# Optimization experiments

Hardware: AMD Instinct MI355X
Metric: run time of the kernel (lower is better)

## Reference

```python
import jax, jax.numpy as jnp
import numpy as np

IMPOSSIBLE = -10000.0
TAGSET_SIZE = 64
NUM_TAGS = TAGSET_SIZE + 2  # C = 66
START_IDX = NUM_TAGS - 2
STOP_IDX = NUM_TAGS - 1
B, L, D = 32, 1024, 1024


def setup_inputs() -> dict:
    key = jax.random.key(0)
    k1, k2, k3, k4, k5 = jax.random.split(key, 5)
    features = jax.random.normal(k1, (B, L, D), dtype=jnp.float32)
    ys = jax.random.randint(k2, (B, L), 0, TAGSET_SIZE).astype(jnp.int64)
    masks = jnp.ones((B, L), dtype=jnp.float32)
    fc_w = jax.random.normal(k3, (D, NUM_TAGS), dtype=jnp.float32) / np.sqrt(D)
    fc_b = jax.random.normal(k4, (NUM_TAGS,), dtype=jnp.float32) * 0.01
    transitions = jax.random.normal(k5, (NUM_TAGS, NUM_TAGS), dtype=jnp.float32)
    # transitions TO start and FROM stop are impossible (torch indexing [to, from])
    transitions = transitions.at[START_IDX, :].set(IMPOSSIBLE)
    transitions = transitions.at[:, STOP_IDX].set(IMPOSSIBLE)
    return {"features": features, "ys": ys, "masks": masks,
            "fc_w": fc_w, "fc_b": fc_b, "transitions": transitions}


def _forward_algorithm(feats, masks, transitions):
    """CRF partition function. feats: [B,L,C], masks: [B,L] -> [B]."""
    Bb, Ll, C = feats.shape
    scores0 = jnp.full((Bb, C), IMPOSSIBLE, dtype=feats.dtype).at[:, START_IDX].set(0.0)

    def step(scores, xs):
        emit_t, m_t = xs  # emit_t: [B,C], m_t: [B]
        # score_t[b, j] = logsumexp_i( scores[b,i] + trans[j,i] + emit[b,j] )
        score_t = jax.nn.logsumexp(
            scores[:, None, :] + transitions[None, :, :] + emit_t[:, :, None], axis=-1)
        scores = score_t * m_t[:, None] + scores * (1.0 - m_t[:, None])
        return scores, None

    xs = (jnp.swapaxes(feats, 0, 1), jnp.swapaxes(masks, 0, 1))  # [L,B,C], [L,B]
    scores, _ = jax.lax.scan(step, scores0, xs)
    return jax.nn.logsumexp(scores + transitions[STOP_IDX][None, :], axis=-1)


def _score_sentence(feats, tags, masks, transitions):
    """Score of the gold tag path. feats: [B,L,C], tags: [B,L] -> [B]."""
    Bb, Ll, C = feats.shape
    emit = jnp.take_along_axis(feats, tags[:, :, None], axis=2)[:, :, 0]  # [B,L]
    start = jnp.full((Bb, 1), START_IDX, dtype=tags.dtype)
    tags_ext = jnp.concatenate([start, tags], axis=1)  # [B,L+1]
    trans_sc = transitions[tags_ext[:, 1:], tags_ext[:, :-1]]  # [B,L]
    lengths = masks.sum(1).astype(jnp.int32)  # [B]
    last_tag = tags_ext[jnp.arange(Bb), lengths]  # [B]
    last_score = transitions[STOP_IDX, last_tag]
    return ((trans_sc + emit) * masks).sum(1) + last_score


def reference(features, ys, masks, fc_w, fc_b, transitions):
    feats = jnp.einsum('bld,dc->blc', features, fc_w) + fc_b  # [B,L,C]
    masks_ = masks.astype(feats.dtype)
    forward_score = _forward_algorithm(feats, masks_, transitions)  # [B]
    gold_score = _score_sentence(feats, ys.astype(jnp.int32), masks_, transitions)  # [B]
    return (forward_score, gold_score)
```

## Files before the change

kernel.cpp:

```cpp
#include <hip/hip_runtime.h>
#include <hip/hip_bf16.h>
#include <stdint.h>


#define START_IDX 64
#define STOP_IDX 65
#define LN2F 0.6931471805599453f

typedef __attribute__((ext_vector_type(4))) float f32x4;
typedef __attribute__((ext_vector_type(8))) __bf16 bf16x8;
typedef __attribute__((ext_vector_type(4))) __bf16 bf16x4;

template <int CTRL>
__device__ __forceinline__ float dpp_mov(float v) {
  return __int_as_float(
      __builtin_amdgcn_update_dpp(0, __float_as_int(v), CTRL, 0xF, 0xF, true));
}
__device__ __forceinline__ float wave_max64(float v) {
  v = fmaxf(v, dpp_mov<0xB1>(v));
  v = fmaxf(v, dpp_mov<0x4E>(v));
  v = fmaxf(v, dpp_mov<0x141>(v));
  v = fmaxf(v, dpp_mov<0x140>(v));
  v = fmaxf(v, dpp_mov<0x142>(v));
  v = fmaxf(v, dpp_mov<0x143>(v));
  return v;
}
__device__ __forceinline__ float wave_sum64(float v) {
  v += dpp_mov<0xB1>(v);
  v += dpp_mov<0x4E>(v);
  v += dpp_mov<0x141>(v);
  v += dpp_mov<0x140>(v);
  v += dpp_mov<0x142>(v);
  v += dpp_mov<0x143>(v);
  return v;
}

__global__ void crf_wcvt(const float* __restrict__ W,
                         unsigned short* __restrict__ Wbt) {
  const int idx = blockIdx.x * 256 + threadIdx.x;
  const int n = idx >> 10, k = idx & 1023;
  union { __bf16 h; unsigned short u; } cv;
  cv.h = (__bf16)W[k * 66 + n];
  Wbt[idx] = cv.u;
}

__global__ __launch_bounds__(256) void crf_fwd(const float* __restrict__ features,
                                               const unsigned short* __restrict__ Wbt,
                                               const float* __restrict__ bias,
                                               const float* __restrict__ masks,
                                               const float* __restrict__ trans,
                                               float* __restrict__ featsOut,
                                               float* __restrict__ chunkP,
                                               int* __restrict__ chunkExp) {
  __shared__ __align__(16) float expE[64][64];
  __shared__ __align__(16) unsigned short T[2][4096];
  __shared__ float wmax[2][4];
  const int tid = threadIdx.x;
  const int w = tid >> 6, lane = tid & 63, g = lane >> 4, q = lane & 15;
  const int c = blockIdx.x, b = blockIdx.y;

  for (int idx = tid; idx < 4096; idx += 256) {
    const int n = idx >> 6, mm = idx & 63;
    const int off = n * 128 + ((2 * mm) ^ ((n & 7) << 4));
    *(unsigned short*)((char*)T[0] + off) =
        (n == mm) ? (unsigned short)0x3F80 : (unsigned short)0;
  }
  if (tid < 4) wmax[0][tid] = 1.0f;

  {
    const int trow = (c << 6) + 16 * w + q;
    const float* Arow = features + ((size_t)b << 20) + (size_t)trow * 1024 + 8 * g;
    const unsigned short* Bp0 = Wbt + (q + 0) * 1024 + 8 * g;
    const unsigned short* Bp1 = Wbt + (q + 16) * 1024 + 8 * g;
    const unsigned short* Bp2 = Wbt + (q + 32) * 1024 + 8 * g;
    const unsigned short* Bp3 = Wbt + (q + 48) * 1024 + 8 * g;
    f32x4 acc0 = {0.f, 0.f, 0.f, 0.f}, acc1 = acc0, acc2 = acc0, acc3 = acc0;
#pragma unroll
    for (int k0 = 0; k0 < 1024; k0 += 32) {
      float4 a0 = *(const float4*)(Arow + k0);
      float4 a1 = *(const float4*)(Arow + k0 + 4);
      bf16x8 af;
      af[0] = (__bf16)a0.x; af[1] = (__bf16)a0.y; af[2] = (__bf16)a0.z; af[3] = (__bf16)a0.w;
      af[4] = (__bf16)a1.x; af[5] = (__bf16)a1.y; af[6] = (__bf16)a1.z; af[7] = (__bf16)a1.w;
      bf16x8 b0 = *(const bf16x8*)(Bp0 + k0);
      bf16x8 b1 = *(const bf16x8*)(Bp1 + k0);
      bf16x8 b2 = *(const bf16x8*)(Bp2 + k0);
      bf16x8 b3 = *(const bf16x8*)(Bp3 + k0);
      acc0 = __builtin_amdgcn_mfma_f32_16x16x32_bf16(af, b0, acc0, 0, 0, 0);
      acc1 = __builtin_amdgcn_mfma_f32_16x16x32_bf16(af, b1, acc1, 0, 0, 0);
      acc2 = __builtin_amdgcn_mfma_f32_16x16x32_bf16(af, b2, acc2, 0, 0, 0);
      acc3 = __builtin_amdgcn_mfma_f32_16x16x32_bf16(af, b3, acc3, 0, 0, 0);
    }
    const float bb0 = bias[q + 0], bb1 = bias[q + 16];
    const float bb2 = bias[q + 32], bb3 = bias[q + 48];
#pragma unroll
    for (int r = 0; r < 4; ++r) {
      const int tl = 16 * w + 4 * g + r;
      float* orow = featsOut + (((size_t)(b << 10) + (c << 6) + tl) << 6) + q;
      const float v0 = acc0[r] + bb0, v1 = acc1[r] + bb1;
      const float v2 = acc2[r] + bb2, v3 = acc3[r] + bb3;
      orow[0] = v0; orow[16] = v1; orow[32] = v2; orow[48] = v3;
      expE[tl][q + 0]  = __expf(v0);
      expE[tl][q + 16] = __expf(v1);
      expE[tl][q + 32] = __expf(v2);
      expE[tl][q + 48] = __expf(v3);
    }
  }

  bf16x8 Ea0, Ea1;
  {
    const int i = 16 * w + q;
    const float* tp0 = trans + i * 66 + 8 * g;
    const float* tp1 = tp0 + 32;
#pragma unroll
    for (int e = 0; e < 8; ++e) {
      Ea0[e] = (__bf16)__expf(tp0[e]);
      Ea1[e] = (__bf16)__expf(tp1[e]);
    }
  }

  float pv[4][4];
#pragma unroll
  for (int nt = 0; nt < 4; ++nt)
#pragma unroll
    for (int r = 0; r < 4; ++r)
      pv[nt][r] = ((16 * w + 4 * g + r) == (q + 16 * nt)) ? 1.f : 0.f;

  const int t0 = (c == 0) ? 1 : (c << 6);
  const int t1 = (c << 6) + 64;
  const float* mb = masks + (b << 10);
  const int tml = t0 + lane;
  const float mkv = mb[tml > 1023 ? 1023 : tml];

  int e_acc = 0;
  int cur = 0;
  __syncthreads();

  for (int t = t0; t < t1; ++t) {
    const int tl = t - (c << 6);
    const float4 ee = *(const float4*)&expE[tl][16 * w + 4 * g];
    const float m =
        __int_as_float(__builtin_amdgcn_readlane(__float_as_int(mkv), t - t0));
    if (m != 0.f) {
      const char* Tb = (const char*)T[cur];
      f32x4 acc[4];
#pragma unroll
      for (int nt = 0; nt < 4; ++nt) {
        const int n = q + 16 * nt;
        const int sw = (n & 7) << 4;
        bf16x8 B0 = *(const bf16x8*)(Tb + n * 128 + ((16 * g) ^ sw));
        bf16x8 B1 = *(const bf16x8*)(Tb + n * 128 + ((64 + 16 * g) ^ sw));
        f32x4 z = {0.f, 0.f, 0.f, 0.f};
        z = __builtin_amdgcn_mfma_f32_16x16x32_bf16(Ea0, B0, z, 0, 0, 0);
        acc[nt] = __builtin_amdgcn_mfma_f32_16x16x32_bf16(Ea1, B1, z, 0, 0, 0);
      }
      const float4 wm = *(const float4*)wmax[cur];
      const float mx = fmaxf(fmaxf(wm.x, wm.y), fmaxf(wm.z, wm.w));
      const int ex = ((__float_as_int(mx) >> 23) & 0xFF) - 127;
      const float sc = __int_as_float((127 - ex) << 23);
      float ce[4];
      ce[0] = ee.x * sc; ce[1] = ee.y * sc; ce[2] = ee.z * sc; ce[3] = ee.w * sc;
      float lm = 0.f;
#pragma unroll
      for (int nt = 0; nt < 4; ++nt) {
#pragma unroll
        for (int r = 0; r < 4; ++r) {
          float val = acc[nt][r] * ce[r];
          if (m != 1.f) val = m * val + (1.f - m) * sc * pv[nt][r];
          pv[nt][r] = val;
          lm = fmaxf(lm, val);
        }
      }
      lm = wave_max64(lm);
      const int nxt = cur ^ 1;
      char* Tw = (char*)T[nxt];
#pragma unroll
      for (int nt = 0; nt < 4; ++nt) {
        bf16x4 o;
        o[0] = (__bf16)pv[nt][0]; o[1] = (__bf16)pv[nt][1];
        o[2] = (__bf16)pv[nt][2]; o[3] = (__bf16)pv[nt][3];
        const int n = q + 16 * nt;
        *(bf16x4*)(Tw + n * 128 + ((32 * w + 8 * g) ^ ((n & 7) << 4))) = o;
      }
      if (lane == 63) wmax[nxt][w] = lm;
      e_acc += ex;
      __syncthreads();
      cur = nxt;
    }
  }

#pragma unroll
  for (int nt = 0; nt < 4; ++nt)
#pragma unroll
    for (int r = 0; r < 4; ++r)
      chunkP[(((size_t)(b * 16 + c)) << 12) + (size_t)(16 * w + 4 * g + r) * 64 +
             q + 16 * nt] = pv[nt][r];
  if (tid == 0) chunkExp[b * 16 + c] = e_acc;
}

__global__ void crf_fin(const float* __restrict__ feats,
                        const int* __restrict__ ys,
                        const float* __restrict__ masks,
                        const float* __restrict__ trans,
                        const float* __restrict__ chunkP,
                        const int* __restrict__ chunkExp,
                        float* __restrict__ out) {
  __shared__ __align__(16) float vb[64];
  const int lane = threadIdx.x;
  const int b = blockIdx.x >> 1;
  if ((blockIdx.x & 1) == 0) {
    float v = __expf(feats[((size_t)b << 16) + lane]) *
              __expf(trans[lane * 66 + START_IDX]);
    int e_acc = 0;
    for (int cc = 0; cc < 16; ++cc) {
      vb[lane] = v;
      __builtin_amdgcn_wave_barrier();
      const float* Pr = chunkP + (((size_t)(b * 16 + cc)) << 12) + (size_t)lane * 64;
      float q0 = 0.f, q1 = 0.f, q2 = 0.f, q3 = 0.f;
#pragma unroll
      for (int j4 = 0; j4 < 16; ++j4) {
        float4 p = *(const float4*)(Pr + 4 * j4);
        float4 x = ((const float4*)vb)[j4];
        q0 = fmaf(p.x, x.x, q0); q1 = fmaf(p.y, x.y, q1);
        q2 = fmaf(p.z, x.z, q2); q3 = fmaf(p.w, x.w, q3);
      }
      const float qq = (q0 + q1) + (q2 + q3);
      float mx = wave_max64(qq);
      mx = __int_as_float(__builtin_amdgcn_readlane(__float_as_int(mx), 63));
      const int ex = ((__float_as_int(mx) >> 23) & 0xFF) - 127;
      v = qq * __int_as_float((127 - ex) << 23);
      e_acc += ex + chunkExp[b * 16 + cc];
      __builtin_amdgcn_wave_barrier();
    }
    const float sum = wave_sum64(v * __expf(trans[STOP_IDX * 66 + lane]));
    const float s =
        __int_as_float(__builtin_amdgcn_readlane(__float_as_int(sum), 63));
    if (lane == 0) out[b] = __logf(s) + (float)e_acc * LN2F;
  } else {
    const float* fb = feats + ((size_t)b << 16);
    const float* mb = masks + (b << 10);
    const int* yb = ys + (b << 10);
    float s = 0.f, cnt = 0.f;
#pragma unroll
    for (int cc = 0; cc < 16; ++cc) {
      const int t = cc * 64 + lane;
      const float m = mb[t];
      const int y = yb[t];
      const int yp = (t == 0) ? START_IDX : yb[t - 1];
      s += (trans[y * 66 + yp] + fb[t * 64 + y]) * m;
      cnt += m;
    }
    float tot = wave_sum64(s);
    float len = wave_sum64(cnt);
    int totb = __builtin_amdgcn_readlane(__float_as_int(tot), 63);
    int lenb = __builtin_amdgcn_readlane(__float_as_int(len), 63);
    if (lane == 0) {
      const int Lr = (int)__int_as_float(lenb);
      const int last = (Lr == 0) ? START_IDX : yb[Lr - 1];
      out[32 + b] = __int_as_float(totb) + trans[STOP_IDX * 66 + last];
    }
  }
}

extern "C" void kernel_launch(void* const* d_in, const int* in_sizes, int n_in,
                              void* d_out, int out_size, void* d_ws, size_t ws_size,
                              hipStream_t stream) {
  const float* features = (const float*)d_in[0];
  const int* ys         = (const int*)d_in[1];
  const float* masks    = (const float*)d_in[2];
  const float* fc_w     = (const float*)d_in[3];
  const float* fc_b     = (const float*)d_in[4];
  const float* trans    = (const float*)d_in[5];
  float* outp = (float*)d_out;

  char* ws = (char*)d_ws;
  float* feats_ws = (float*)ws;
  unsigned short* Wbt = (unsigned short*)(ws + 8388608);
  float* chunkP = (float*)(ws + 8388608 + 131072);
  int* chunkExp = (int*)(ws + 8388608 + 131072 + 8388608);

  crf_wcvt<<<256, 256, 0, stream>>>(fc_w, Wbt);
  dim3 cg(16, 32);
  crf_fwd<<<cg, 256, 0, stream>>>(features, Wbt, fc_b, masks, trans,
                                  feats_ws, chunkP, chunkExp);
  crf_fin<<<64, 64, 0, stream>>>(feats_ws, ys, masks, trans, chunkP, chunkExp, outp);
}
```

Before: 285.9 us.

## Stage GEMM operands through LDS with direct global-to-LDS loads and swizzle

The projection GEMM in crf_fwd now stages 64-wide K slices of features and bf16 weights into swizzled shared memory using global_load_lds, then reads MFMA fragments from LDS, instead of each lane loading its fragments straight from global memory. The weight conversion kernel is rewritten as a tiled transpose through shared memory so both reads and writes are coalesced, and the identity-matrix init of T is simplified. The aim is better coalescing and fewer scattered global loads. In exchange it uses more LDS per block and adds two barriers per K step with no double buffering, which may reduce occupancy and overlap.

```diff
diff --git a/kernel.cpp b/kernel.cpp
--- a/kernel.cpp
+++ b/kernel.cpp
@@ -10,6 +10,12 @@
 typedef __attribute__((ext_vector_type(4))) float f32x4;
 typedef __attribute__((ext_vector_type(8))) __bf16 bf16x8;
 typedef __attribute__((ext_vector_type(4))) __bf16 bf16x4;
+
+__device__ __forceinline__ void gload_lds16(const void* g, void* l) {
+  __builtin_amdgcn_global_load_lds(
+      (const __attribute__((address_space(1))) void*)g,
+      (__attribute__((address_space(3))) void*)l, 16, 0, 0);
+}
 
 template <int CTRL>
 __device__ __forceinline__ float dpp_mov(float v) {
@@ -35,13 +41,26 @@
   return v;
 }
 
-__global__ void crf_wcvt(const float* __restrict__ W,
-                         unsigned short* __restrict__ Wbt) {
-  const int idx = blockIdx.x * 256 + threadIdx.x;
-  const int n = idx >> 10, k = idx & 1023;
-  union { __bf16 h; unsigned short u; } cv;
-  cv.h = (__bf16)W[k * 66 + n];
-  Wbt[idx] = cv.u;
+__global__ __launch_bounds__(256) void crf_wcvt(const float* __restrict__ W,
+                                                unsigned short* __restrict__ Wbt) {
+  __shared__ float tile[64][65];
+  const int t = threadIdx.x;
+  const int kb = blockIdx.x;
+#pragma unroll
+  for (int i = 0; i < 16; ++i) {
+    const int f = i * 256 + t;
+    const int k = f >> 6, n = f & 63;
+    tile[k][n] = W[(kb * 64 + k) * 66 + n];
+  }
+  __syncthreads();
+#pragma unroll
+  for (int i = 0; i < 16; ++i) {
+    const int f = i * 256 + t;
+    const int n = f >> 6, k = f & 63;
+    union { __bf16 h; unsigned short u; } cv;
+    cv.h = (__bf16)tile[k][n];
+    Wbt[n * 1024 + kb * 64 + k] = cv.u;
+  }
 }
 
 __global__ __launch_bounds__(256) void crf_fwd(const float* __restrict__ features,
@@ -52,6 +71,8 @@
                                                float* __restrict__ featsOut,
                                                float* __restrict__ chunkP,
                                                int* __restrict__ chunkExp) {
+  __shared__ __align__(16) float As[4096];
+  __shared__ __align__(16) unsigned short Bs[4096];
   __shared__ __align__(16) float expE[64][64];
   __shared__ __align__(16) unsigned short T[2][4096];
   __shared__ float wmax[2][4];
@@ -59,37 +80,60 @@
   const int w = tid >> 6, lane = tid & 63, g = lane >> 4, q = lane & 15;
   const int c = blockIdx.x, b = blockIdx.y;
 
-  for (int idx = tid; idx < 4096; idx += 256) {
-    const int n = idx >> 6, mm = idx & 63;
-    const int off = n * 128 + ((2 * mm) ^ ((n & 7) << 4));
-    *(unsigned short*)((char*)T[0] + off) =
-        (n == mm) ? (unsigned short)0x3F80 : (unsigned short)0;
-  }
-  if (tid < 4) wmax[0][tid] = 1.0f;
-
   {
-    const int trow = (c << 6) + 16 * w + q;
-    const float* Arow = features + ((size_t)b << 20) + (size_t)trow * 1024 + 8 * g;
-    const unsigned short* Bp0 = Wbt + (q + 0) * 1024 + 8 * g;
-    const unsigned short* Bp1 = Wbt + (q + 16) * 1024 + 8 * g;
-    const unsigned short* Bp2 = Wbt + (q + 32) * 1024 + 8 * g;
-    const unsigned short* Bp3 = Wbt + (q + 48) * 1024 + 8 * g;
-    f32x4 acc0 = {0.f, 0.f, 0.f, 0.f}, acc1 = acc0, acc2 = acc0, acc3 = acc0;
-#pragma unroll
-    for (int k0 = 0; k0 < 1024; k0 += 32) {
-      float4 a0 = *(const float4*)(Arow + k0);
-      float4 a1 = *(const float4*)(Arow + k0 + 4);
-      bf16x8 af;
-      af[0] = (__bf16)a0.x; af[1] = (__bf16)a0.y; af[2] = (__bf16)a0.z; af[3] = (__bf16)a0.w;
-      af[4] = (__bf16)a1.x; af[5] = (__bf16)a1.y; af[6] = (__bf16)a1.z; af[7] = (__bf16)a1.w;
-      bf16x8 b0 = *(const bf16x8*)(Bp0 + k0);
-      bf16x8 b1 = *(const bf16x8*)(Bp1 + k0);
-      bf16x8 b2 = *(const bf16x8*)(Bp2 + k0);
-      bf16x8 b3 = *(const bf16x8*)(Bp3 + k0);
-      acc0 = __builtin_amdgcn_mfma_f32_16x16x32_bf16(af, b0, acc0, 0, 0, 0);
-      acc1 = __builtin_amdgcn_mfma_f32_16x16x32_bf16(af, b1, acc1, 0, 0, 0);
-      acc2 = __builtin_amdgcn_mfma_f32_16x16x32_bf16(af, b2, acc2, 0, 0, 0);
-      acc3 = __builtin_amdgcn_mfma_f32_16x16x32_bf16(af, b3, acc3, 0, 0, 0);
+    f32x4 z4 = {0.f, 0.f, 0.f, 0.f};
+    *(f32x4*)((char*)T[0] + tid * 16) = z4;
+    *(f32x4*)((char*)T[0] + 4096 + tid * 16) = z4;
+    __syncthreads();
+    if (tid < 64) {
+      const int off = tid * 128 + ((2 * tid) ^ ((tid & 7) << 4));
+      *(unsigned short*)((char*)T[0] + off) = (unsigned short)0x3F80;
+    }
+    if (tid < 4) wmax[0][tid] = 1.0f;
+  }
+
+  {
+    const float* Abase = features + ((size_t)b << 20) + ((size_t)(c << 6) << 10);
+    f32x4 acc[4];
+#pragma unroll
+    for (int nt = 0; nt < 4; ++nt) acc[nt] = (f32x4){0.f, 0.f, 0.f, 0.f};
+
+    const int sA = (q & 7) << 4;
+    for (int k0 = 0; k0 < 1024; k0 += 64) {
+#pragma unroll
+      for (int j = 0; j < 4; ++j) {
+        const int row = 16 * w + 4 * j + (lane >> 4);
+        const int colb = ((lane & 15) * 16) ^ ((row & 7) << 4);
+        gload_lds16((const char*)(Abase + (size_t)row * 1024 + k0) + colb,
+                    (char*)As + (16 * w + 4 * j) * 256);
+      }
+#pragma unroll
+      for (int j = 0; j < 2; ++j) {
+        const int n = 16 * w + 8 * j + (lane >> 3);
+        const int colb = ((lane & 7) * 16) ^ ((n & 7) << 4);
+        gload_lds16((const char*)(Wbt + (size_t)n * 1024 + k0) + colb,
+                    (char*)Bs + (16 * w + 8 * j) * 128);
+      }
+      __syncthreads();
+#pragma unroll
+      for (int kk = 0; kk < 64; kk += 32) {
+        const char* Ab = (const char*)As + (16 * w + q) * 256;
+        float4 alo = *(const float4*)(Ab + ((kk * 4 + 32 * g) ^ sA));
+        float4 ahi = *(const float4*)(Ab + ((kk * 4 + 32 * g + 16) ^ sA));
+        bf16x8 af;
+        af[0] = (__bf16)alo.x; af[1] = (__bf16)alo.y;
+        af[2] = (__bf16)alo.z; af[3] = (__bf16)alo.w;
+        af[4] = (__bf16)ahi.x; af[5] = (__bf16)ahi.y;
+        af[6] = (__bf16)ahi.z; af[7] = (__bf16)ahi.w;
+#pragma unroll
+        for (int nt = 0; nt < 4; ++nt) {
+          const int n = q + 16 * nt;
+          bf16x8 bf = *(const bf16x8*)((const char*)Bs + n * 128 +
+                                       ((kk * 2 + 16 * g) ^ ((n & 7) << 4)));
+          acc[nt] = __builtin_amdgcn_mfma_f32_16x16x32_bf16(af, bf, acc[nt], 0, 0, 0);
+        }
+      }
+      __syncthreads();
     }
     const float bb0 = bias[q + 0], bb1 = bias[q + 16];
     const float bb2 = bias[q + 32], bb3 = bias[q + 48];
@@ -97,8 +141,8 @@
     for (int r = 0; r < 4; ++r) {
       const int tl = 16 * w + 4 * g + r;
       float* orow = featsOut + (((size_t)(b << 10) + (c << 6) + tl) << 6) + q;
-      const float v0 = acc0[r] + bb0, v1 = acc1[r] + bb1;
-      const float v2 = acc2[r] + bb2, v3 = acc3[r] + bb3;
+      const float v0 = acc[0][r] + bb0, v1 = acc[1][r] + bb1;
+      const float v2 = acc[2][r] + bb2, v3 = acc[3][r] + bb3;
       orow[0] = v0; orow[16] = v1; orow[32] = v2; orow[48] = v3;
       expE[tl][q + 0]  = __expf(v0);
       expE[tl][q + 16] = __expf(v1);
@@ -279,7 +323,7 @@
   float* chunkP = (float*)(ws + 8388608 + 131072);
   int* chunkExp = (int*)(ws + 8388608 + 131072 + 8388608);
 
-  crf_wcvt<<<256, 256, 0, stream>>>(fc_w, Wbt);
+  crf_wcvt<<<16, 256, 0, stream>>>(fc_w, Wbt);
   dim3 cg(16, 32);
   crf_fwd<<<cg, 256, 0, stream>>>(features, Wbt, fc_b, masks, trans,
                                   feats_ws, chunkP, chunkExp);
```

After: 274.8 us. 1.04x faster.
